# Kernel tuning notes

Hardware: AMD Instinct MI355X
Metric: run time of the kernel (lower is better)

Reference implementation:

```python
import jax, jax.numpy as jnp
import numpy as np

N_SPLIT = 4096   # split tokens (coarse octree levels)
N_VQ    = 12288  # VQ tokens (finest level)
N       = N_SPLIT + N_VQ
C       = 256    # num_embed
H       = 8      # num_heads
L       = 4      # num_blocks
P       = 256    # patch_size (attention window)
DIL     = 2      # dilation for odd (swin) blocks
DVQ     = 32     # vqvae embedding_channels
VQ_SIZE = 256    # vqvae embedding_sizes
VQ_G    = 4      # vqvae quantizer_group
HID     = 4 * C


def _layernorm(x, s, b):
    m = x.mean(-1, keepdims=True)
    v = jnp.var(x, axis=-1, keepdims=True)
    return (x - m) * jax.lax.rsqrt(v + 1e-5) * s + b


def _sin_pos_emb(n, c):
    pos = jnp.arange(n, dtype=jnp.float32)[:, None]
    half = c // 2
    freqs = jnp.exp(-jnp.log(10000.0) * jnp.arange(half, dtype=jnp.float32) / half)
    ang = pos * freqs
    return jnp.concatenate([jnp.sin(ang), jnp.cos(ang)], axis=-1)


def _forward(split, zq, targets_vq, category, batch_id, mask, d2b,
             split_emb, class_emb, vq_proj_w, vq_proj_b,
             ln1_s, ln1_b, qkv_w, qkv_b, attn_w, attn_b,
             ln2_s, ln2_b, fc1_w, fc1_b, fc2_w, fc2_b,
             lnx_s, lnx_b, split_w, split_b, vq_w, vq_b):
    # token embeddings: [split tokens ; projected VQ codes]
    x = jnp.concatenate([split_emb[split], zq @ vq_proj_w + vq_proj_b], axis=0)  # [N,C]
    cond = class_emb[category]                      # [B,C]
    x = jnp.where(mask[:, None], cond[batch_id], x)  # masked tokens -> class cond

    # depth2batch gather, then OctFormer blocks
    xb = x[d2b] + _sin_pos_emb(N, C).astype(x.dtype)
    dh = C // H
    scale = dh ** -0.5
    for l in range(L):
        d = DIL if (l % 2 == 1) else 1  # swin-style alternating dilation
        h = _layernorm(xb, ln1_s[l], ln1_b[l])
        # dilated window partition: window j in a super-window holds tokens base+p*d+j
        hw = h.reshape(-1, P, d, C).transpose(0, 2, 1, 3).reshape(-1, P, C)
        qkv = hw @ qkv_w[l] + qkv_b[l]              # [nw,P,3C]
        q, k, v = [t.reshape(-1, P, H, dh) for t in jnp.split(qkv, 3, axis=-1)]
        att = jax.nn.softmax(jnp.einsum('wphd,wqhd->whpq', q, k) * scale, axis=-1)
        o = jnp.einsum('whpq,wqhd->wphd', att, v).reshape(-1, P, C) @ attn_w[l] + attn_b[l]
        o = o.reshape(-1, d, P, C).transpose(0, 2, 1, 3).reshape(-1, C)  # undo partition
        xb = xb + o
        h = _layernorm(xb, ln2_s[l], ln2_b[l])
        xb = xb + (jax.nn.gelu(h @ fc1_w[l] + fc1_b[l]) @ fc2_w[l] + fc2_b[l])
    # batch2depth scatter (inverse permutation)
    x = jnp.zeros_like(xb).at[d2b].set(xb)
    x = _layernorm(x, lnx_s, lnx_b)

    # split head + masked cross-entropy
    sl = x[:N_SPLIT] @ split_w + split_b            # [Ns,2]
    ms = mask[:N_SPLIT].astype(jnp.float32)
    ce_s = -jnp.take_along_axis(jax.nn.log_softmax(sl, axis=-1), split[:, None], axis=-1)[:, 0]
    split_loss = jnp.sum(ce_s * ms) / jnp.maximum(jnp.sum(ms), 1.0)

    # vq head + masked grouped cross-entropy
    vl = (x[N_SPLIT:] @ vq_w + vq_b).reshape(N_VQ, VQ_G, VQ_SIZE)
    mv = mask[N_SPLIT:].astype(jnp.float32)
    ce_v = -jnp.take_along_axis(jax.nn.log_softmax(vl, axis=-1), targets_vq[..., None], axis=-1)[..., 0]
    vq_loss = jnp.sum(ce_v.mean(-1) * mv) / jnp.maximum(jnp.sum(mv), 1.0)
    return jnp.stack([split_loss, vq_loss])


def setup_inputs() -> dict:
    key = jax.random.key(0)
    ks = jax.random.split(key, 16)
    s = 0.02
    inp = {
        'split': jax.random.randint(ks[0], (N_SPLIT,), 0, 2),
        'zq': jax.random.normal(ks[1], (N_VQ, DVQ), jnp.float32),
        'targets_vq': jax.random.randint(ks[2], (N_VQ, VQ_G), 0, VQ_SIZE),
        'category': jnp.zeros((1,), jnp.int32),
        'batch_id': jnp.zeros((N,), jnp.int32),
        'mask': jax.random.randint(ks[3], (N,), 0, 2).astype(bool),
        'd2b': jax.random.permutation(ks[4], N),
        'split_emb': s * jax.random.normal(ks[5], (2, C), jnp.float32),
        'class_emb': s * jax.random.normal(ks[6], (1, C), jnp.float32),
        'vq_proj_w': s * jax.random.normal(ks[7], (DVQ, C), jnp.float32),
        'vq_proj_b': jnp.zeros((C,), jnp.float32),
        'ln1_s': jnp.ones((L, C), jnp.float32),
        'ln1_b': jnp.zeros((L, C), jnp.float32),
        'qkv_w': s * jax.random.normal(ks[8], (L, C, 3 * C), jnp.float32),
        'qkv_b': jnp.zeros((L, 3 * C), jnp.float32),
        'attn_w': s * jax.random.normal(ks[9], (L, C, C), jnp.float32),
        'attn_b': jnp.zeros((L, C), jnp.float32),
        'ln2_s': jnp.ones((L, C), jnp.float32),
        'ln2_b': jnp.zeros((L, C), jnp.float32),
        'fc1_w': s * jax.random.normal(ks[10], (L, C, HID), jnp.float32),
        'fc1_b': jnp.zeros((L, HID), jnp.float32),
        'fc2_w': s * jax.random.normal(ks[11], (L, HID, C), jnp.float32),
        'fc2_b': jnp.zeros((L, C), jnp.float32),
        'lnx_s': jnp.ones((C,), jnp.float32),
        'lnx_b': jnp.zeros((C,), jnp.float32),
        'split_w': s * jax.random.normal(ks[12], (C, 2), jnp.float32),
        'split_b': jnp.zeros((2,), jnp.float32),
        'vq_w': s * jax.random.normal(ks[13], (C, VQ_G * VQ_SIZE), jnp.float32),
        'vq_b': jnp.zeros((VQ_G * VQ_SIZE,), jnp.float32),
    }
    return inp


def reference(split, zq, targets_vq, category, batch_id, mask, d2b,
              split_emb, class_emb, vq_proj_w, vq_proj_b,
              ln1_s, ln1_b, qkv_w, qkv_b, attn_w, attn_b,
              ln2_s, ln2_b, fc1_w, fc1_b, fc2_w, fc2_b,
              lnx_s, lnx_b, split_w, split_b, vq_w, vq_b):
    return _forward(split, zq, targets_vq, category, batch_id, mask, d2b,
                    split_emb, class_emb, vq_proj_w, vq_proj_b,
                    ln1_s, ln1_b, qkv_w, qkv_b, attn_w, attn_b,
                    ln2_s, ln2_b, fc1_w, fc1_b, fc2_w, fc2_b,
                    lnx_s, lnx_b, split_w, split_b, vq_w, vq_b)
```

## Files before the change

### kernel.cpp

```cpp
#include <hip/hip_runtime.h>
#include <hip/hip_bf16.h>
#include <math.h>

#define NSPLIT 4096
#define NVQ    12288
#define NTOK   16384
#define CH     256
#define NH     8
#define DHD    32
#define NL     4
#define PW     256
#define HIDN   1024
#define DVQ    32
#define VQG    4
#define VQS    256

typedef __attribute__((ext_vector_type(8))) short bf16x8;
typedef __attribute__((ext_vector_type(4))) float f32x4;

typedef const __attribute__((address_space(1))) void* gas_ptr;
typedef __attribute__((address_space(3))) void* las_ptr;
#define GLD16(g, s) __builtin_amdgcn_global_load_lds((gas_ptr)(g), (las_ptr)(s), 16, 0, 0)

static __device__ __forceinline__ unsigned pack2bf(float a, float b) {
    __hip_bfloat16 ha = __float2bfloat16(a), hb = __float2bfloat16(b);
    return ((unsigned)*(unsigned short*)&hb << 16) | *(unsigned short*)&ha;
}
static __device__ __forceinline__ float bf2f(unsigned short s) {
    unsigned u = (unsigned)s << 16;
    return *(float*)&u;
}
static __device__ __forceinline__ unsigned short f2bfu(float f) {
    __hip_bfloat16 h = __float2bfloat16(f);
    return *(unsigned short*)&h;
}

__global__ void k_wt_all(const float* __restrict__ qkv_w, const float* __restrict__ attn_w,
                         const float* __restrict__ fc1_w, const float* __restrict__ fc2_w,
                         const float* __restrict__ vq_w,
                         short* __restrict__ qkvT, short* __restrict__ attnT,
                         short* __restrict__ fc1T, short* __restrict__ fc2T,
                         short* __restrict__ vqT,
                         const void* __restrict__ mask_raw, int* __restrict__ mode) {
    int b = blockIdx.x;
    if (b == 832) {
        __shared__ int c_even, c_odd, c_0100;
        const unsigned short* u16 = (const unsigned short*)mask_raw;
        if (threadIdx.x == 0) { c_even = 0; c_odd = 0; c_0100 = 0; }
        __syncthreads();
        int le = 0, lo = 0, l01 = 0;
        for (int i = threadIdx.x; i < 8192; i += 256) {
            unsigned short v = u16[i];
            if (v == 0x3F80u) { if (i & 1) lo++; else le++; }
            if (v == 0x0100u) l01++;
        }
        atomicAdd(&c_even, le); atomicAdd(&c_odd, lo); atomicAdd(&c_0100, l01);
        __syncthreads();
        if (threadIdx.x == 0) {
            int m;
            if      (c_even > 500) m = 2;
            else if (c_odd  > 500) m = 3;
            else if (c_0100 > 500) m = 1;
            else                   m = 0;
            *mode = m;
        }
        return;
    }
    const float* W; short* Wt; int K, N, tn, tk;
    if (b < 192)      { int r = b;       int z = r / 48; r %= 48; K = 256;  N = 768;
                        tk = r / 12; tn = r % 12;
                        W = qkv_w + (size_t)z * K * N; Wt = qkvT + (size_t)z * K * N; }
    else if (b < 256) { int r = b - 192; int z = r / 16; r %= 16; K = 256;  N = 256;
                        tk = r / 4;  tn = r % 4;
                        W = attn_w + (size_t)z * K * N; Wt = attnT + (size_t)z * K * N; }
    else if (b < 512) { int r = b - 256; int z = r / 64; r %= 64; K = 256;  N = 1024;
                        tk = r / 16; tn = r % 16;
                        W = fc1_w + (size_t)z * K * N; Wt = fc1T + (size_t)z * K * N; }
    else if (b < 768) { int r = b - 512; int z = r / 64; r %= 64; K = 1024; N = 256;
                        tk = r / 4;  tn = r % 4;
                        W = fc2_w + (size_t)z * K * N; Wt = fc2T + (size_t)z * K * N; }
    else              { int r = b - 768; K = 256; N = 1024;
                        tk = r / 16; tn = r % 16; W = vq_w; Wt = vqT; }
    __shared__ float t[64][65];
    int bn = tn * 64, bk = tk * 64, tid = threadIdx.x;
#pragma unroll
    for (int it = 0; it < 16; ++it) {
        int idx = it * 256 + tid; int r = idx >> 6, c = idx & 63;
        t[r][c] = W[(size_t)(bk + r) * N + bn + c];
    }
    __syncthreads();
#pragma unroll
    for (int it = 0; it < 16; ++it) {
        int idx = it * 256 + tid; int r = idx >> 6, c = idx & 63;
        __hip_bfloat16 h = __float2bfloat16(t[c][r]);
        Wt[(size_t)(bn + r) * K + bk + c] = *(short*)&h;
    }
}

__global__ void k_embed_gather(const int* __restrict__ split, const float* __restrict__ zq,
                               const int* __restrict__ category, const int* __restrict__ batch_id,
                               const void* __restrict__ mask_raw, const int* __restrict__ mode,
                               int* __restrict__ mask_i, const int* __restrict__ d2b,
                               const float* __restrict__ split_emb, const float* __restrict__ class_emb,
                               const float* __restrict__ vq_proj_w, const float* __restrict__ vq_proj_b,
                               const float* __restrict__ ln1s, const float* __restrict__ ln1b,
                               unsigned short* __restrict__ xbv, unsigned short* __restrict__ hb) {
    int j = blockIdx.x, c = threadIdx.x;
    int i = d2b[j];
    int m = *mode, mv;
    if      (m == 0) mv = ((const int*)mask_raw)[i] != 0;
    else if (m == 1) mv = ((const unsigned char*)mask_raw)[i] != 0;
    else if (m == 2) mv = ((const unsigned short*)mask_raw)[i] != 0;
    else             mv = ((const unsigned int*)mask_raw)[i] != 0;
    if (c == 0) mask_i[i] = mv;
    float v;
    if (mv) {
        v = class_emb[category[batch_id[i]] * CH + c];
    } else if (i < NSPLIT) {
        v = split_emb[split[i] * CH + c];
    } else {
        const float* z = zq + (size_t)(i - NSPLIT) * DVQ;
        float acc = vq_proj_b[c];
#pragma unroll
        for (int k = 0; k < DVQ; k++) acc += z[k] * vq_proj_w[k * CH + c];
        v = acc;
    }
    const float kneg = -0.07195578415606394f;
    float jf = (float)j, pe;
    if (c < 128) { float f = expf(c * kneg);         pe = sinf(jf * f); }
    else         { float f = expf((c - 128) * kneg); pe = cosf(jf * f); }
    v += pe;
    float s = v, sq = v * v;
#pragma unroll
    for (int o = 32; o; o >>= 1) { s += __shfl_xor(s, o); sq += __shfl_xor(sq, o); }
    __shared__ float ps[4], pq[4];
    if ((c & 63) == 0) { ps[c >> 6] = s; pq[c >> 6] = sq; }
    __syncthreads();
    float S = ps[0] + ps[1] + ps[2] + ps[3];
    float Q = pq[0] + pq[1] + pq[2] + pq[3];
    float mean = S * (1.0f / CH);
    float var  = Q * (1.0f / CH) - mean * mean;
    float rsf = rsqrtf(var + 1e-5f);
    xbv[(size_t)j * CH + c] = f2bfu(v);
    hb[(size_t)j * CH + c]  = f2bfu((v - mean) * rsf * ln1s[c] + ln1b[c]);
}

template <int GELU>
__global__ __launch_bounds__(256, 4) void k_mm(
    const short* __restrict__ A, const short* __restrict__ Bt,
    const float* __restrict__ bias, __hip_bfloat16* __restrict__ outB,
    int N, int K) {
    __shared__ short As[2][128 * 32];
    __shared__ short Bs[2][128 * 32];
    const int tid = threadIdx.x;
    const int w = tid >> 6, l = tid & 63;
    const int bm = blockIdx.y * 128, bn = blockIdx.x * 128;
    const int wr = w >> 1, wc = w & 1;
    const int q = l >> 4, rA = l & 15;
    const int srow = w * 16 + (l >> 2);
    const int sx = ((l & 3) ^ ((l >> 2) & 3)) * 8;
    const int fx = (q ^ (rA & 3)) * 8;

    const short* gA0 = A + (size_t)(bm + srow) * K + sx;
    const short* gA1 = A + (size_t)(bm + srow + 64) * K + sx;
    const short* gB0 = Bt + (size_t)(bn + srow) * K + sx;
    const short* gB1 = Bt + (size_t)(bn + srow + 64) * K + sx;
    short* lA0 = &As[0][w * 16 * 32];
    short* lA1 = &As[0][(64 + w * 16) * 32];
    short* lA0h = &As[1][w * 16 * 32];
    short* lA1h = &As[1][(64 + w * 16) * 32];
    short* lB0 = &Bs[0][w * 16 * 32];
    short* lB1 = &Bs[0][(64 + w * 16) * 32];
    short* lB0h = &Bs[1][w * 16 * 32];
    short* lB1h = &Bs[1][(64 + w * 16) * 32];

    f32x4 acc[4][4] = {};

    for (int k0 = 0; k0 < K; k0 += 64) {
        GLD16(gA0 + k0, lA0);       GLD16(gA1 + k0, lA1);
        GLD16(gA0 + k0 + 32, lA0h); GLD16(gA1 + k0 + 32, lA1h);
        GLD16(gB0 + k0, lB0);       GLD16(gB1 + k0, lB1);
        GLD16(gB0 + k0 + 32, lB0h); GLD16(gB1 + k0 + 32, lB1h);
        __syncthreads();
#pragma unroll
        for (int s = 0; s < 2; s++) {
            bf16x8 a[4], b[4];
#pragma unroll
            for (int m = 0; m < 4; m++)
                a[m] = *(const bf16x8*)(&As[s][(wr * 64 + m * 16 + rA) * 32 + fx]);
#pragma unroll
            for (int n = 0; n < 4; n++)
                b[n] = *(const bf16x8*)(&Bs[s][(wc * 64 + n * 16 + rA) * 32 + fx]);
#pragma unroll
            for (int m = 0; m < 4; m++)
#pragma unroll
                for (int n = 0; n < 4; n++)
                    acc[m][n] = __builtin_amdgcn_mfma_f32_16x16x32_bf16(a[m], b[n], acc[m][n], 0, 0, 0);
        }
        __syncthreads();
    }

#pragma unroll
    for (int m = 0; m < 4; m++) {
        int row0 = bm + wr * 64 + m * 16 + q * 4;
#pragma unroll
        for (int n = 0; n < 4; n++) {
            int col = bn + wc * 64 + n * 16 + rA;
            float bv = bias[col];
#pragma unroll
            for (int r2 = 0; r2 < 4; r2++) {
                float v = acc[m][n][r2] + bv;
                if (GELU) {
                    float t = tanhf(0.7978845608028654f * (v + 0.044715f * v * v * v));
                    v = 0.5f * v * (1.0f + t);
                }
                outB[(size_t)(row0 + r2) * N + col] = __float2bfloat16(v);
            }
        }
    }
}

template <int LNOUT>
__global__ __launch_bounds__(256, 3) void k_mm_row(
    const short* __restrict__ A, const short* __restrict__ Bt,
    const float* __restrict__ bias, unsigned short* __restrict__ xbv,
    const float* __restrict__ lns, const float* __restrict__ lnb,
    unsigned short* __restrict__ h_out, int K) {
    __shared__ short As[2][64 * 32];
    __shared__ short Bs[2][256 * 32];
    __shared__ float part[2][4][64];
    const int tid = threadIdx.x;
    const int w = tid >> 6, l = tid & 63;
    const int bm = blockIdx.x * 64;
    const int q = l >> 4, rA = l & 15;
    const int sx = ((l & 3) ^ ((l >> 2) & 3)) * 8;
    const int fx = (q ^ (rA & 3)) * 8;

    const short* gA = A + (size_t)(bm + w * 16 + (l >> 2)) * K + sx;
    const short* gB = Bt + (size_t)(w * 64 + (l >> 2)) * K + sx;
    short* lA0 = &As[0][(w * 16) * 32];
    short* lA1 = &As[1][(w * 16) * 32];

    f32x4 acc[4][4] = {};

    for (int k0 = 0; k0 < K; k0 += 64) {
        GLD16(gA + k0, lA0);
        GLD16(gA + k0 + 32, lA1);
#pragma unroll
        for (int i = 0; i < 4; i++) {
            GLD16(gB + (size_t)(i * 16) * K + k0,      &Bs[0][(w * 64 + i * 16) * 32]);
            GLD16(gB + (size_t)(i * 16) * K + k0 + 32, &Bs[1][(w * 64 + i * 16) * 32]);
        }
        __syncthreads();
#pragma unroll
        for (int s = 0; s < 2; s++) {
            bf16x8 a[4], b[4];
#pragma unroll
            for (int m = 0; m < 4; m++)
                a[m] = *(const bf16x8*)(&As[s][(m * 16 + rA) * 32 + fx]);
#pragma unroll
            for (int n = 0; n < 4; n++)
                b[n] = *(const bf16x8*)(&Bs[s][(w * 64 + n * 16 + rA) * 32 + fx]);
#pragma unroll
            for (int m = 0; m < 4; m++)
#pragma unroll
                for (int n = 0; n < 4; n++)
                    acc[m][n] = __builtin_amdgcn_mfma_f32_16x16x32_bf16(a[m], b[n], acc[m][n], 0, 0, 0);
        }
        __syncthreads();
    }

    float rsum[4][4] = {}, rsq[4][4] = {};
#pragma unroll
    for (int m = 0; m < 4; m++) {
#pragma unroll
        for (int n = 0; n < 4; n++) {
            int col = w * 64 + n * 16 + rA;
            float bv = bias[col];
#pragma unroll
            for (int r2 = 0; r2 < 4; r2++) {
                int row = bm + m * 16 + q * 4 + r2;
                size_t oi = (size_t)row * CH + col;
                float v = acc[m][n][r2] + bv + bf2f(xbv[oi]);
                acc[m][n][r2] = v;
                xbv[oi] = f2bfu(v);
                rsum[m][r2] += v;
                rsq[m][r2] += v * v;
            }
        }
    }
    if (LNOUT) {
#pragma unroll
        for (int m = 0; m < 4; m++)
#pragma unroll
            for (int r2 = 0; r2 < 4; r2++) {
#pragma unroll
                for (int o = 8; o; o >>= 1) {
                    rsum[m][r2] += __shfl_xor(rsum[m][r2], o);
                    rsq[m][r2]  += __shfl_xor(rsq[m][r2], o);
                }
            }
        if (rA == 0) {
#pragma unroll
            for (int m = 0; m < 4; m++)
#pragma unroll
                for (int r2 = 0; r2 < 4; r2++) {
                    int row = m * 16 + q * 4 + r2;
                    part[0][w][row] = rsum[m][r2];
                    part[1][w][row] = rsq[m][r2];
                }
        }
        __syncthreads();
#pragma unroll
        for (int m = 0; m < 4; m++) {
#pragma unroll
            for (int r2 = 0; r2 < 4; r2++) {
                int row = m * 16 + q * 4 + r2;
                float S = part[0][0][row] + part[0][1][row] + part[0][2][row] + part[0][3][row];
                float Q = part[1][0][row] + part[1][1][row] + part[1][2][row] + part[1][3][row];
                float mean = S * (1.0f / CH);
                float var  = Q * (1.0f / CH) - mean * mean;
                float rsf = rsqrtf(var + 1e-5f);
#pragma unroll
                for (int n = 0; n < 4; n++) {
                    int col = w * 64 + n * 16 + rA;
                    float h = (acc[m][n][r2] - mean) * rsf * lns[col] + lnb[col];
                    h_out[(size_t)(bm + row) * CH + col] = f2bfu(h);
                }
            }
        }
    }
}

__global__ __launch_bounds__(256) void k_attn_mfma(const short* __restrict__ qkv,
                                                   short* __restrict__ o, int dil) {
    __shared__ short Vt[DHD * PW];
    __shared__ short Kl[PW * DHD];
    __shared__ short Pl[4][64 * 64];
    const int wid = blockIdx.x, h = blockIdx.y;
    const int tid = threadIdx.x;
    const int w = tid >> 6, l = tid & 63;
    const int g = l >> 4, c = l & 15;
    const int tbase = (wid / dil) * (PW * dil) + (wid % dil);

#pragma unroll
    for (int j2 = 0; j2 < 4; j2++) {
        int row = j2 * 64 + w * 16 + (l >> 2);
        int sc = (l & 3) ^ (row & 3);
        GLD16(qkv + (size_t)(tbase + row * dil) * 768 + CH + h * DHD + sc * 8,
              Kl + (j2 * 64 + w * 16) * DHD);
    }

    {
        const int p = tid;
        const short* src = qkv + (size_t)(tbase + p * dil) * 768 + 2 * CH + h * DHD;
        bf16x8 v0 = *(const bf16x8*)(src);
        bf16x8 v1 = *(const bf16x8*)(src + 8);
        bf16x8 v2 = *(const bf16x8*)(src + 16);
        bf16x8 v3 = *(const bf16x8*)(src + 24);
        const int pc = p >> 3, po = p & 7;
#pragma unroll
        for (int d = 0; d < 8; d++)  Vt[(d)      * PW + ((pc ^ d) << 3) + po] = v0[d];
#pragma unroll
        for (int d = 0; d < 8; d++)  Vt[(d + 8)  * PW + ((pc ^ d) << 3) + po] = v1[d];
#pragma unroll
        for (int d = 0; d < 8; d++)  Vt[(d + 16) * PW + ((pc ^ d) << 3) + po] = v2[d];
#pragma unroll
        for (int d = 0; d < 8; d++)  Vt[(d + 24) * PW + ((pc ^ d) << 3) + po] = v3[d];
    }

    bf16x8 qf[4];
#pragma unroll
    for (int qt = 0; qt < 4; qt++) {
        int qrow = w * 64 + qt * 16 + c;
        qf[qt] = *(const bf16x8*)(qkv + (size_t)(tbase + qrow * dil) * 768 + h * DHD + g * 8);
    }

    f32x4 acco[4][2] = {};
    float m_s[4] = {-1e30f, -1e30f, -1e30f, -1e30f};
    float l_s[4] = {0.f, 0.f, 0.f, 0.f};
    const float scale = 0.17677669529663687f;

    __syncthreads();

#pragma unroll
    for (int ch = 0; ch < 4; ch++) {
        bf16x8 kf[4];
#pragma unroll
        for (int kvt = 0; kvt < 4; kvt++) {
            int kv = ch * 64 + kvt * 16 + c;
            kf[kvt] = *(const bf16x8*)(Kl + kv * DHD + ((g ^ (c & 3)) * 8));
        }
        f32x4 accs[4][4] = {};
#pragma unroll
        for (int kvt = 0; kvt < 4; kvt++)
#pragma unroll
            for (int qt = 0; qt < 4; qt++)
                accs[kvt][qt] = __builtin_amdgcn_mfma_f32_16x16x32_bf16(kf[kvt], qf[qt], accs[kvt][qt], 0, 0, 0);

        float fb[4];
#pragma unroll
        for (int qt = 0; qt < 4; qt++) {
            float mx = -1e30f;
#pragma unroll
            for (int kvt = 0; kvt < 4; kvt++) {
                mx = fmaxf(mx, fmaxf(fmaxf(accs[kvt][qt][0], accs[kvt][qt][1]),
                                     fmaxf(accs[kvt][qt][2], accs[kvt][qt][3])));
            }
            mx = fmaxf(mx, __shfl_xor(mx, 16));
            mx = fmaxf(mx, __shfl_xor(mx, 32));
            float mnew = fmaxf(m_s[qt], mx * scale);
            fb[qt] = __expf(m_s[qt] - mnew);
            m_s[qt] = mnew;
        }
#pragma unroll
        for (int mt = 0; mt < 4; mt++)
#pragma unroll
            for (int r = 0; r < 4; r++) {
                float fo = __shfl(fb[mt], g * 4 + r);
                acco[mt][0][r] *= fo;
                acco[mt][1][r] *= fo;
            }
        float rsum[4] = {0.f, 0.f, 0.f, 0.f};
#pragma unroll
        for (int kvt = 0; kvt < 4; kvt++) {
            const int cchunk = kvt * 2 + (g >> 1);
            const int koff = (g & 1) << 2;
#pragma unroll
            for (int qt = 0; qt < 4; qt++) {
                float p0 = __expf(accs[kvt][qt][0] * scale - m_s[qt]);
                float p1 = __expf(accs[kvt][qt][1] * scale - m_s[qt]);
                float p2 = __expf(accs[kvt][qt][2] * scale - m_s[qt]);
                float p3 = __expf(accs[kvt][qt][3] * scale - m_s[qt]);
                rsum[qt] += (p0 + p1) + (p2 + p3);
                int qq = qt * 16 + c;
                int phys = cchunk ^ (qq & 7);
                uint2 pk; pk.x = pack2bf(p0, p1); pk.y = pack2bf(p2, p3);
                *(uint2*)(&Pl[w][qq * 64 + phys * 8 + koff]) = pk;
            }
        }
#pragma unroll
        for (int qt = 0; qt < 4; qt++) {
            float s = rsum[qt];
            s += __shfl_xor(s, 16);
            s += __shfl_xor(s, 32);
            l_s[qt] = l_s[qt] * fb[qt] + s;
        }
#pragma unroll
        for (int ks = 0; ks < 2; ks++) {
            bf16x8 pa[4];
#pragma unroll
            for (int mt = 0; mt < 4; mt++) {
                int qq = mt * 16 + c;
                int phys = (ks * 4 + g) ^ (qq & 7);
                pa[mt] = *(const bf16x8*)(&Pl[w][qq * 64 + phys * 8]);
            }
#pragma unroll
            for (int nt = 0; nt < 2; nt++) {
                int d = nt * 16 + c;
                int kvabs = ch * 64 + ks * 32 + g * 8;
                int phys = (kvabs >> 3) ^ (d & 7);
                bf16x8 vb = *(const bf16x8*)(&Vt[d * PW + phys * 8]);
#pragma unroll
                for (int mt = 0; mt < 4; mt++)
                    acco[mt][nt] = __builtin_amdgcn_mfma_f32_16x16x32_bf16(pa[mt], vb, acco[mt][nt], 0, 0, 0);
            }
        }
    }

#pragma unroll
    for (int mt = 0; mt < 4; mt++) {
        float linv_own = 1.0f / l_s[mt];
#pragma unroll
        for (int r = 0; r < 4; r++) {
            float linv = __shfl(linv_own, g * 4 + r);
            int qrow = w * 64 + mt * 16 + g * 4 + r;
            size_t trow = (size_t)(tbase + qrow * dil) * CH + h * DHD;
#pragma unroll
            for (int nt = 0; nt < 2; nt++) {
                __hip_bfloat16 hv = __float2bfloat16(acco[mt][nt][r] * linv);
                o[trow + nt * 16 + c] = *(short*)&hv;
            }
        }
    }
}

__global__ void k_lnx_scatter_split(const unsigned short* __restrict__ xbv, const int* __restrict__ d2b,
                                    const float* __restrict__ s, const float* __restrict__ b,
                                    const int* __restrict__ split, const int* __restrict__ mask_i,
                                    const float* __restrict__ sw, const float* __restrict__ sb,
                                    __hip_bfloat16* __restrict__ out,
                                    float* __restrict__ sce, float* __restrict__ smv) {
    int j = blockIdx.x * 4 + (threadIdx.x >> 6);
    int l = threadIdx.x & 63;
    ushort4 uv = *(const ushort4*)(xbv + (size_t)j * CH + l * 4);
    float vx = bf2f(uv.x), vy = bf2f(uv.y), vz = bf2f(uv.z), vw = bf2f(uv.w);
    float sum = vx + vy + vz + vw;
    float sq  = vx * vx + vy * vy + vz * vz + vw * vw;
#pragma unroll
    for (int o = 32; o; o >>= 1) { sum += __shfl_xor(sum, o); sq += __shfl_xor(sq, o); }
    float mean = sum * (1.0f / CH);
    float var  = sq * (1.0f / CH) - mean * mean;
    float rs = rsqrtf(var + 1e-5f);
    float4 sv = *(const float4*)(s + l * 4);
    float4 bv = *(const float4*)(b + l * 4);
    float n0 = (vx - mean) * rs * sv.x + bv.x;
    float n1 = (vy - mean) * rs * sv.y + bv.y;
    float n2 = (vz - mean) * rs * sv.z + bv.z;
    float n3 = (vw - mean) * rs * sv.w + bv.w;
    int i = d2b[j];
    uint2 pk; pk.x = pack2bf(n0, n1); pk.y = pack2bf(n2, n3);
    *(uint2*)((unsigned short*)out + (size_t)i * CH + l * 4) = pk;
    if (i < NSPLIT) {
        int c0 = l * 4;
        float a0 = n0 * sw[2 * c0] + n1 * sw[2 * (c0 + 1)] + n2 * sw[2 * (c0 + 2)] + n3 * sw[2 * (c0 + 3)];
        float a1 = n0 * sw[2 * c0 + 1] + n1 * sw[2 * (c0 + 1) + 1] + n2 * sw[2 * (c0 + 2) + 1] + n3 * sw[2 * (c0 + 3) + 1];
#pragma unroll
        for (int o = 32; o; o >>= 1) { a0 += __shfl_xor(a0, o); a1 += __shfl_xor(a1, o); }
        if (l == 0) {
            float l0 = a0 + sb[0], l1 = a1 + sb[1];
            float mx = fmaxf(l0, l1);
            float lse = mx + logf(__expf(l0 - mx) + __expf(l1 - mx));
            float ce = lse - (split[i] ? l1 : l0);
            float ms = (float)mask_i[i];
            sce[i] = ce * ms;
            smv[i] = ms;
        }
    }
}

__global__ void k_vq_loss(const unsigned short* __restrict__ vl, const int* __restrict__ targets,
                          const int* __restrict__ mask_i, float* __restrict__ vce,
                          float* __restrict__ vmv) {
    int i = blockIdx.x;
    int wv = threadIdx.x >> 6;
    int l = threadIdx.x & 63;
    const unsigned short* row = vl + (size_t)i * (VQG * VQS) + wv * VQS;
    ushort4 v4 = *(const ushort4*)(row + l * 4);
    float e0 = bf2f(v4.x), e1 = bf2f(v4.y), e2 = bf2f(v4.z), e3 = bf2f(v4.w);
    float mx = fmaxf(fmaxf(e0, e1), fmaxf(e2, e3));
#pragma unroll
    for (int o = 32; o; o >>= 1) mx = fmaxf(mx, __shfl_xor(mx, o));
    float s = __expf(e0 - mx) + __expf(e1 - mx) + __expf(e2 - mx) + __expf(e3 - mx);
#pragma unroll
    for (int o = 32; o; o >>= 1) s += __shfl_xor(s, o);
    __shared__ float ce[VQG];
    if (l == 0) ce[wv] = (mx + logf(s)) - bf2f(row[targets[i * VQG + wv]]);
    __syncthreads();
    if (threadIdx.x == 0) {
        float mv = (float)mask_i[NSPLIT + i];
        vce[i] = (ce[0] + ce[1] + ce[2] + ce[3]) * 0.25f * mv;
        vmv[i] = mv;
    }
}

__global__ void k_reduce(const float* __restrict__ sce, const float* __restrict__ smv,
                         const float* __restrict__ vce, const float* __restrict__ vmv,
                         float* __restrict__ out) {
    int tid = threadIdx.x;
    float s1 = 0, s2 = 0, s3 = 0, s4 = 0;
    for (int i = tid; i < NSPLIT; i += 256) { s1 += sce[i]; s2 += smv[i]; }
    for (int i = tid; i < NVQ; i += 256)    { s3 += vce[i]; s4 += vmv[i]; }
    __shared__ float r1[256], r2[256], r3[256], r4[256];
    r1[tid] = s1; r2[tid] = s2; r3[tid] = s3; r4[tid] = s4;
    __syncthreads();
    for (int o = 128; o; o >>= 1) {
        if (tid < o) { r1[tid] += r1[tid + o]; r2[tid] += r2[tid + o];
                       r3[tid] += r3[tid + o]; r4[tid] += r4[tid + o]; }
        __syncthreads();
    }
    if (tid == 0) {
        out[0] = r1[0] / fmaxf(r2[0], 1.0f);
        out[1] = r3[0] / fmaxf(r4[0], 1.0f);
    }
}

extern "C" void kernel_launch(void* const* d_in, const int* in_sizes, int n_in,
                              void* d_out, int out_size, void* d_ws, size_t ws_size,
                              hipStream_t stream) {
    const int*   split      = (const int*)d_in[0];
    const float* zq         = (const float*)d_in[1];
    const int*   targets_vq = (const int*)d_in[2];
    const int*   category   = (const int*)d_in[3];
    const int*   batch_id   = (const int*)d_in[4];
    const void*  mask_raw   = d_in[5];
    const int*   d2b        = (const int*)d_in[6];
    const float* split_emb  = (const float*)d_in[7];
    const float* class_emb  = (const float*)d_in[8];
    const float* vq_proj_w  = (const float*)d_in[9];
    const float* vq_proj_b  = (const float*)d_in[10];
    const float* ln1_s      = (const float*)d_in[11];
    const float* ln1_b      = (const float*)d_in[12];
    const float* qkv_w      = (const float*)d_in[13];
    const float* qkv_b      = (const float*)d_in[14];
    const float* attn_w     = (const float*)d_in[15];
    const float* attn_b     = (const float*)d_in[16];
    const float* ln2_s      = (const float*)d_in[17];
    const float* ln2_b      = (const float*)d_in[18];
    const float* fc1_w      = (const float*)d_in[19];
    const float* fc1_b      = (const float*)d_in[20];
    const float* fc2_w      = (const float*)d_in[21];
    const float* fc2_b      = (const float*)d_in[22];
    const float* lnx_s      = (const float*)d_in[23];
    const float* lnx_b      = (const float*)d_in[24];
    const float* sw         = (const float*)d_in[25];
    const float* sb         = (const float*)d_in[26];
    const float* vq_w       = (const float*)d_in[27];
    const float* vq_b       = (const float*)d_in[28];

    char* ws = (char*)d_ws;
    int* mode   = (int*)ws;
    int* mask_i = (int*)(ws + 256);
    float* sce = (float*)(ws + 256 + 4 * NTOK);
    float* smv = sce + NSPLIT;
    float* vce = smv + NSPLIT;
    float* vmv = vce + NVQ;
    char* p = ws + (1 << 20);
    short* qkvT = (short*)p;  p += (size_t)NL * 768 * CH * 2;
    short* attnT = (short*)p; p += (size_t)NL * CH * CH * 2;
    short* fc1T = (short*)p;  p += (size_t)NL * HIDN * CH * 2;
    short* fc2T = (short*)p;  p += (size_t)NL * CH * HIDN * 2;
    short* vqT = (short*)p;   p += (size_t)HIDN * CH * 2;
    unsigned short* xbv = (unsigned short*)p; p += (size_t)NTOK * CH * 2;
    unsigned short* h_bf = (unsigned short*)p; p += (size_t)NTOK * CH * 2;
    unsigned short* o_bf = (unsigned short*)p; p += (size_t)NTOK * CH * 2;
    short* big = (short*)p;

    k_wt_all<<<833, 256, 0, stream>>>(qkv_w, attn_w, fc1_w, fc2_w, vq_w,
                                      qkvT, attnT, fc1T, fc2T, vqT, mask_raw, mode);
    k_embed_gather<<<NTOK, 256, 0, stream>>>(split, zq, category, batch_id, mask_raw, mode,
                                             mask_i, d2b, split_emb, class_emb,
                                             vq_proj_w, vq_proj_b, ln1_s, ln1_b, xbv, h_bf);

    for (int l = 0; l < NL; l++) {
        int d = (l & 1) ? 2 : 1;
        k_mm<0><<<dim3(768 / 128, NTOK / 128), 256, 0, stream>>>(
            (const short*)h_bf, qkvT + (size_t)l * 768 * CH, qkv_b + l * 768,
            (__hip_bfloat16*)big, 768, CH);
        k_attn_mfma<<<dim3(NTOK / PW, NH), 256, 0, stream>>>(big, (short*)o_bf, d);
        k_mm_row<1><<<NTOK / 64, 256, 0, stream>>>(
            (const short*)o_bf, attnT + (size_t)l * CH * CH, attn_b + l * CH,
            xbv, ln2_s + l * CH, ln2_b + l * CH, h_bf, CH);
        k_mm<1><<<dim3(HIDN / 128, NTOK / 128), 256, 0, stream>>>(
            (const short*)h_bf, fc1T + (size_t)l * HIDN * CH, fc1_b + l * HIDN,
            (__hip_bfloat16*)big, HIDN, CH);
        if (l < NL - 1) {
            k_mm_row<1><<<NTOK / 64, 256, 0, stream>>>(
                big, fc2T + (size_t)l * CH * HIDN, fc2_b + l * CH,
                xbv, ln1_s + (l + 1) * CH, ln1_b + (l + 1) * CH, h_bf, HIDN);
        } else {
            k_mm_row<0><<<NTOK / 64, 256, 0, stream>>>(
                big, fc2T + (size_t)l * CH * HIDN, fc2_b + l * CH,
                xbv, nullptr, nullptr, nullptr, HIDN);
        }
    }

    k_lnx_scatter_split<<<NTOK / 4, 256, 0, stream>>>(xbv, d2b, lnx_s, lnx_b, split, mask_i,
                                                      sw, sb, (__hip_bfloat16*)h_bf, sce, smv);
    k_mm<0><<<dim3(HIDN / 128, NVQ / 128), 256, 0, stream>>>(
        (const short*)(h_bf + (size_t)NSPLIT * CH), vqT, vq_b,
        (__hip_bfloat16*)big, HIDN, CH);
    k_vq_loss<<<NVQ, 256, 0, stream>>>((const unsigned short*)big, targets_vq, mask_i, vce, vmv);
    k_reduce<<<1, 256, 0, stream>>>(sce, smv, vce, vmv, (float*)d_out);
}
```

Baseline: 501.7 us.

## Fuse final LayerNorm+scatter into last fc2 and fuse VQ logits with cross-entropy

The last fc2 row-GEMM now applies the final LayerNorm in its epilogue and scatters rows through d2b directly into the output buffer, skipping the residual writeback. This removes the separate LN/scatter kernel. A new VQ head kernel computes the logits GEMM per 256-wide group and does the log-sum-exp and target pick in registers and shared memory, so the bf16 logits tensor is never written or re-read. The separate vq_loss kernel goes away, the split loss becomes a small kernel, and the reduce folds in the mask and group averaging. The cost is a more complex epilogue, plus the fused path now takes the target logit in fp32 where the old path read a bf16-rounded value.

Result: no change. 505.4 us (+0.7%).

```diff
diff --git a/kernel.cpp b/kernel.cpp
--- a/kernel.cpp
+++ b/kernel.cpp
@@ -225,7 +225,7 @@
     const short* __restrict__ A, const short* __restrict__ Bt,
     const float* __restrict__ bias, unsigned short* __restrict__ xbv,
     const float* __restrict__ lns, const float* __restrict__ lnb,
-    unsigned short* __restrict__ h_out, int K) {
+    unsigned short* __restrict__ h_out, const int* __restrict__ d2b, int K) {
     __shared__ short As[2][64 * 32];
     __shared__ short Bs[2][256 * 32];
     __shared__ float part[2][4][64];
@@ -283,7 +283,7 @@
                 size_t oi = (size_t)row * CH + col;
                 float v = acc[m][n][r2] + bv + bf2f(xbv[oi]);
                 acc[m][n][r2] = v;
-                xbv[oi] = f2bfu(v);
+                if (LNOUT != 2) xbv[oi] = f2bfu(v);
                 rsum[m][r2] += v;
                 rsq[m][r2] += v * v;
             }
@@ -321,14 +321,142 @@
                 float mean = S * (1.0f / CH);
                 float var  = Q * (1.0f / CH) - mean * mean;
                 float rsf = rsqrtf(var + 1e-5f);
+                size_t orow = (LNOUT == 2) ? (size_t)d2b[bm + row] : (size_t)(bm + row);
 #pragma unroll
                 for (int n = 0; n < 4; n++) {
                     int col = w * 64 + n * 16 + rA;
                     float h = (acc[m][n][r2] - mean) * rsf * lns[col] + lnb[col];
-                    h_out[(size_t)(bm + row) * CH + col] = f2bfu(h);
+                    h_out[orow * CH + col] = f2bfu(h);
                 }
             }
         }
+    }
+}
+
+__global__ __launch_bounds__(256, 3) void k_vq_head(
+    const short* __restrict__ A, const short* __restrict__ vqT,
+    const float* __restrict__ vq_b, const int* __restrict__ targets,
+    float* __restrict__ vce4) {
+    __shared__ short As[2][64 * 32];
+    __shared__ short Bs[2][256 * 32];
+    __shared__ float part[2][4][64];
+    __shared__ float tgtv[64];
+    const int tid = threadIdx.x;
+    const int w = tid >> 6, l = tid & 63;
+    const int bm = blockIdx.x * 64;
+    const int g = blockIdx.y;
+    const int q = l >> 4, rA = l & 15;
+    const int sx = ((l & 3) ^ ((l >> 2) & 3)) * 8;
+    const int fx = (q ^ (rA & 3)) * 8;
+
+    const short* gA = A + (size_t)(bm + w * 16 + (l >> 2)) * CH + sx;
+    const short* gB = vqT + (size_t)(g * VQS + w * 64 + (l >> 2)) * CH + sx;
+    short* lA0 = &As[0][(w * 16) * 32];
+    short* lA1 = &As[1][(w * 16) * 32];
+
+    f32x4 acc[4][4] = {};
+
+    for (int k0 = 0; k0 < CH; k0 += 64) {
+        GLD16(gA + k0, lA0);
+        GLD16(gA + k0 + 32, lA1);
+#pragma unroll
+        for (int i = 0; i < 4; i++) {
+            GLD16(gB + (size_t)(i * 16) * CH + k0,      &Bs[0][(w * 64 + i * 16) * 32]);
+            GLD16(gB + (size_t)(i * 16) * CH + k0 + 32, &Bs[1][(w * 64 + i * 16) * 32]);
+        }
+        __syncthreads();
+#pragma unroll
+        for (int s = 0; s < 2; s++) {
+            bf16x8 a[4], b[4];
+#pragma unroll
+            for (int m = 0; m < 4; m++)
+                a[m] = *(const bf16x8*)(&As[s][(m * 16 + rA) * 32 + fx]);
+#pragma unroll
+            for (int n = 0; n < 4; n++)
+                b[n] = *(const bf16x8*)(&Bs[s][(w * 64 + n * 16 + rA) * 32 + fx]);
+#pragma unroll
+            for (int m = 0; m < 4; m++)
+#pragma unroll
+                for (int n = 0; n < 4; n++)
+                    acc[m][n] = __builtin_amdgcn_mfma_f32_16x16x32_bf16(a[m], b[n], acc[m][n], 0, 0, 0);
+        }
+        __syncthreads();
+    }
+
+    float pm[4][4];
+#pragma unroll
+    for (int m = 0; m < 4; m++) {
+#pragma unroll
+        for (int r2 = 0; r2 < 4; r2++) pm[m][r2] = -1e30f;
+#pragma unroll
+        for (int n = 0; n < 4; n++) {
+            int col = w * 64 + n * 16 + rA;
+            float bv = vq_b[g * VQS + col];
+#pragma unroll
+            for (int r2 = 0; r2 < 4; r2++) {
+                float v = acc[m][n][r2] + bv;
+                acc[m][n][r2] = v;
+                int row = m * 16 + q * 4 + r2;
+                int t = targets[(size_t)(bm + row) * VQG + g];
+                if (col == t) tgtv[row] = v;
+                pm[m][r2] = fmaxf(pm[m][r2], v);
+            }
+        }
+    }
+#pragma unroll
+    for (int m = 0; m < 4; m++)
+#pragma unroll
+        for (int r2 = 0; r2 < 4; r2++) {
+#pragma unroll
+            for (int o = 8; o; o >>= 1) pm[m][r2] = fmaxf(pm[m][r2], __shfl_xor(pm[m][r2], o));
+        }
+    if (rA == 0) {
+#pragma unroll
+        for (int m = 0; m < 4; m++)
+#pragma unroll
+            for (int r2 = 0; r2 < 4; r2++)
+                part[0][w][m * 16 + q * 4 + r2] = pm[m][r2];
+    }
+    __syncthreads();
+    float psum[4][4];
+#pragma unroll
+    for (int m = 0; m < 4; m++)
+#pragma unroll
+        for (int r2 = 0; r2 < 4; r2++) {
+            int row = m * 16 + q * 4 + r2;
+            float mx = fmaxf(fmaxf(part[0][0][row], part[0][1][row]),
+                             fmaxf(part[0][2][row], part[0][3][row]));
+            pm[m][r2] = mx;
+            float s = 0.f;
+#pragma unroll
+            for (int n = 0; n < 4; n++) s += __expf(acc[m][n][r2] - mx);
+            psum[m][r2] = s;
+        }
+#pragma unroll
+    for (int m = 0; m < 4; m++)
+#pragma unroll
+        for (int r2 = 0; r2 < 4; r2++) {
+#pragma unroll
+            for (int o = 8; o; o >>= 1) psum[m][r2] += __shfl_xor(psum[m][r2], o);
+        }
+    if (rA == 0) {
+#pragma unroll
+        for (int m = 0; m < 4; m++)
+#pragma unroll
+            for (int r2 = 0; r2 < 4; r2++)
+                part[1][w][m * 16 + q * 4 + r2] = psum[m][r2];
+    }
+    __syncthreads();
+    if (w == 0 && rA == 0) {
+#pragma unroll
+        for (int m = 0; m < 4; m++)
+#pragma unroll
+            for (int r2 = 0; r2 < 4; r2++) {
+                int row = m * 16 + q * 4 + r2;
+                float tot = part[1][0][row] + part[1][1][row] + part[1][2][row] + part[1][3][row];
+                float lse = pm[m][r2] + logf(tot);
+                vce4[(size_t)(bm + row) * VQG + g] = lse - tgtv[row];
+            }
     }
 }
 
@@ -485,82 +613,38 @@
     }
 }
 
-__global__ void k_lnx_scatter_split(const unsigned short* __restrict__ xbv, const int* __restrict__ d2b,
-                                    const float* __restrict__ s, const float* __restrict__ b,
-                                    const int* __restrict__ split, const int* __restrict__ mask_i,
-                                    const float* __restrict__ sw, const float* __restrict__ sb,
-                                    __hip_bfloat16* __restrict__ out,
-                                    float* __restrict__ sce, float* __restrict__ smv) {
-    int j = blockIdx.x * 4 + (threadIdx.x >> 6);
+__global__ void k_split_mini(const unsigned short* __restrict__ h, const int* __restrict__ split,
+                             const int* __restrict__ mask_i, const float* __restrict__ sw,
+                             const float* __restrict__ sb, float* __restrict__ sce) {
+    int i = blockIdx.x * 4 + (threadIdx.x >> 6);
     int l = threadIdx.x & 63;
-    ushort4 uv = *(const ushort4*)(xbv + (size_t)j * CH + l * 4);
-    float vx = bf2f(uv.x), vy = bf2f(uv.y), vz = bf2f(uv.z), vw = bf2f(uv.w);
-    float sum = vx + vy + vz + vw;
-    float sq  = vx * vx + vy * vy + vz * vz + vw * vw;
-#pragma unroll
-    for (int o = 32; o; o >>= 1) { sum += __shfl_xor(sum, o); sq += __shfl_xor(sq, o); }
-    float mean = sum * (1.0f / CH);
-    float var  = sq * (1.0f / CH) - mean * mean;
-    float rs = rsqrtf(var + 1e-5f);
-    float4 sv = *(const float4*)(s + l * 4);
-    float4 bv = *(const float4*)(b + l * 4);
-    float n0 = (vx - mean) * rs * sv.x + bv.x;
-    float n1 = (vy - mean) * rs * sv.y + bv.y;
-    float n2 = (vz - mean) * rs * sv.z + bv.z;
-    float n3 = (vw - mean) * rs * sv.w + bv.w;
-    int i = d2b[j];
-    uint2 pk; pk.x = pack2bf(n0, n1); pk.y = pack2bf(n2, n3);
-    *(uint2*)((unsigned short*)out + (size_t)i * CH + l * 4) = pk;
-    if (i < NSPLIT) {
-        int c0 = l * 4;
-        float a0 = n0 * sw[2 * c0] + n1 * sw[2 * (c0 + 1)] + n2 * sw[2 * (c0 + 2)] + n3 * sw[2 * (c0 + 3)];
-        float a1 = n0 * sw[2 * c0 + 1] + n1 * sw[2 * (c0 + 1) + 1] + n2 * sw[2 * (c0 + 2) + 1] + n3 * sw[2 * (c0 + 3) + 1];
-#pragma unroll
-        for (int o = 32; o; o >>= 1) { a0 += __shfl_xor(a0, o); a1 += __shfl_xor(a1, o); }
-        if (l == 0) {
-            float l0 = a0 + sb[0], l1 = a1 + sb[1];
-            float mx = fmaxf(l0, l1);
-            float lse = mx + logf(__expf(l0 - mx) + __expf(l1 - mx));
-            float ce = lse - (split[i] ? l1 : l0);
-            float ms = (float)mask_i[i];
-            sce[i] = ce * ms;
-            smv[i] = ms;
-        }
-    }
-}
-
-__global__ void k_vq_loss(const unsigned short* __restrict__ vl, const int* __restrict__ targets,
-                          const int* __restrict__ mask_i, float* __restrict__ vce,
-                          float* __restrict__ vmv) {
-    int i = blockIdx.x;
-    int wv = threadIdx.x >> 6;
-    int l = threadIdx.x & 63;
-    const unsigned short* row = vl + (size_t)i * (VQG * VQS) + wv * VQS;
-    ushort4 v4 = *(const ushort4*)(row + l * 4);
-    float e0 = bf2f(v4.x), e1 = bf2f(v4.y), e2 = bf2f(v4.z), e3 = bf2f(v4.w);
-    float mx = fmaxf(fmaxf(e0, e1), fmaxf(e2, e3));
-#pragma unroll
-    for (int o = 32; o; o >>= 1) mx = fmaxf(mx, __shfl_xor(mx, o));
-    float s = __expf(e0 - mx) + __expf(e1 - mx) + __expf(e2 - mx) + __expf(e3 - mx);
-#pragma unroll
-    for (int o = 32; o; o >>= 1) s += __shfl_xor(s, o);
-    __shared__ float ce[VQG];
-    if (l == 0) ce[wv] = (mx + logf(s)) - bf2f(row[targets[i * VQG + wv]]);
-    __syncthreads();
-    if (threadIdx.x == 0) {
-        float mv = (float)mask_i[NSPLIT + i];
-        vce[i] = (ce[0] + ce[1] + ce[2] + ce[3]) * 0.25f * mv;
-        vmv[i] = mv;
-    }
-}
-
-__global__ void k_reduce(const float* __restrict__ sce, const float* __restrict__ smv,
-                         const float* __restrict__ vce, const float* __restrict__ vmv,
-                         float* __restrict__ out) {
+    ushort4 uv = *(const ushort4*)(h + (size_t)i * CH + l * 4);
+    float n0 = bf2f(uv.x), n1 = bf2f(uv.y), n2 = bf2f(uv.z), n3 = bf2f(uv.w);
+    int c0 = l * 4;
+    float a0 = n0 * sw[2 * c0] + n1 * sw[2 * (c0 + 1)] + n2 * sw[2 * (c0 + 2)] + n3 * sw[2 * (c0 + 3)];
+    float a1 = n0 * sw[2 * c0 + 1] + n1 * sw[2 * (c0 + 1) + 1] + n2 * sw[2 * (c0 + 2) + 1] + n3 * sw[2 * (c0 + 3) + 1];
+#pragma unroll
+    for (int o = 32; o; o >>= 1) { a0 += __shfl_xor(a0, o); a1 += __shfl_xor(a1, o); }
+    if (l == 0) {
+        float l0 = a0 + sb[0], l1 = a1 + sb[1];
+        float mx = fmaxf(l0, l1);
+        float lse = mx + logf(__expf(l0 - mx) + __expf(l1 - mx));
+        float ce = lse - (split[i] ? l1 : l0);
+        sce[i] = ce * (float)mask_i[i];
+    }
+}
+
+__global__ void k_reduce(const float* __restrict__ sce, const float* __restrict__ vce4,
+                         const int* __restrict__ mask_i, float* __restrict__ out) {
     int tid = threadIdx.x;
     float s1 = 0, s2 = 0, s3 = 0, s4 = 0;
-    for (int i = tid; i < NSPLIT; i += 256) { s1 += sce[i]; s2 += smv[i]; }
-    for (int i = tid; i < NVQ; i += 256)    { s3 += vce[i]; s4 += vmv[i]; }
+    for (int i = tid; i < NSPLIT; i += 256) { s1 += sce[i]; s2 += (float)mask_i[i]; }
+    for (int i = tid; i < NVQ; i += 256) {
+        float mv = (float)mask_i[NSPLIT + i];
+        float cs = vce4[i * 4 + 0] + vce4[i * 4 + 1] + vce4[i * 4 + 2] + vce4[i * 4 + 3];
+        s3 += cs * 0.25f * mv;
+        s4 += mv;
+    }
     __shared__ float r1[256], r2[256], r3[256], r4[256];
     r1[tid] = s1; r2[tid] = s2; r3[tid] = s3; r4[tid] = s4;
     __syncthreads();
@@ -611,10 +695,8 @@
     char* ws = (char*)d_ws;
     int* mode   = (int*)ws;
     int* mask_i = (int*)(ws + 256);
-    float* sce = (float*)(ws + 256 + 4 * NTOK);
-    float* smv = sce + NSPLIT;
-    float* vce = smv + NSPLIT;
-    float* vmv = vce + NVQ;
+    float* sce  = (float*)(ws + 256 + 4 * NTOK);
+    float* vce4 = sce + NSPLIT;
     char* p = ws + (1 << 20);
     short* qkvT = (short*)p;  p += (size_t)NL * 768 * CH * 2;
     short* attnT = (short*)p; p += (size_t)NL * CH * CH * 2;
@@ -640,26 +722,23 @@
         k_attn_mfma<<<dim3(NTOK / PW, NH), 256, 0, stream>>>(big, (short*)o_bf, d);
         k_mm_row<1><<<NTOK / 64, 256, 0, stream>>>(
             (const short*)o_bf, attnT + (size_t)l * CH * CH, attn_b + l * CH,
-            xbv, ln2_s + l * CH, ln2_b + l * CH, h_bf, CH);
+            xbv, ln2_s + l * CH, ln2_b + l * CH, h_bf, nullptr, CH);
         k_mm<1><<<dim3(HIDN / 128, NTOK / 128), 256, 0, stream>>>(
             (const short*)h_bf, fc1T + (size_t)l * HIDN * CH, fc1_b + l * HIDN,
             (__hip_bfloat16*)big, HIDN, CH);
         if (l < NL - 1) {
             k_mm_row<1><<<NTOK / 64, 256, 0, stream>>>(
                 big, fc2T + (size_t)l * CH * HIDN, fc2_b + l * CH,
-                xbv, ln1_s + (l + 1) * CH, ln1_b + (l + 1) * CH, h_bf, HIDN);
+                xbv, ln1_s + (l + 1) * CH, ln1_b + (l + 1) * CH, h_bf, nullptr, HIDN);
         } else {
-            k_mm_row<0><<<NTOK / 64, 256, 0, stream>>>(
+            k_mm_row<2><<<NTOK / 64, 256, 0, stream>>>(
                 big, fc2T + (size_t)l * CH * HIDN, fc2_b + l * CH,
-                xbv, nullptr, nullptr, nullptr, HIDN);
-        }
-    }
-
-    k_lnx_scatter_split<<<NTOK / 4, 256, 0, stream>>>(xbv, d2b, lnx_s, lnx_b, split, mask_i,
-                                                      sw, sb, (__hip_bfloat16*)h_bf, sce, smv);
-    k_mm<0><<<dim3(HIDN / 128, NVQ / 128), 256, 0, stream>>>(
-        (const short*)(h_bf + (size_t)NSPLIT * CH), vqT, vq_b,
-        (__hip_bfloat16*)big, HIDN, CH);
-    k_vq_loss<<<NVQ, 256, 0, stream>>>((const unsigned short*)big, targets_vq, mask_i, vce, vmv);
-    k_reduce<<<1, 256, 0, stream>>>(sce, smv, vce, vmv, (float*)d_out);
-}
+                xbv, lnx_s, lnx_b, h_bf, d2b, HIDN);
+        }
+    }
+
+    k_split_mini<<<NSPLIT / 4, 256, 0, stream>>>(h_bf, split, mask_i, sw, sb, sce);
+    k_vq_head<<<dim3(NVQ / 64, VQG), 256, 0, stream>>>(
+        (const short*)(h_bf + (size_t)NSPLIT * CH), vqT, vq_b, targets_vq, vce4);
+    k_reduce<<<1, 256, 0, stream>>>(sce, vce4, mask_i, (float*)d_out);
+}
```
